# Optimization experiments

Measured on AMD Instinct MI355X. Metric: run time of the kernel, lower is better.

## Reference

```python
import jax, jax.numpy as jnp
import numpy as np

N = 50000       # nodes
E = 1600000     # edges (avg degree 32)
IN = 64         # in_channels
ED = 16         # edge_dim
H = 128         # hidden_channels


def setup_inputs() -> dict:
    key = jax.random.key(0)
    ks = jax.random.split(key, 32)
    rn = lambda k, shape, s: jax.random.normal(k, shape, jnp.float32) * s
    inp = {}
    inp['x'] = rn(ks[0], (N, IN), 1.0)
    inp['edge_index'] = jax.random.randint(ks[1], (2, E), 0, N, dtype=jnp.int64)
    inp['edge_attr'] = rn(ks[2], (E, ED), 1.0)
    # per-layer params: edge linear (ED -> node_dim), MLP (d_in->H, H->H)
    node_dims = [IN, H, H]
    i = 3
    for l, d in enumerate(node_dims):
        inp[f'We{l}'] = rn(ks[i], (ED, d), 1.0 / np.sqrt(ED)); i += 1
        inp[f'be{l}'] = jnp.zeros((d,), jnp.float32)
        inp[f'W1_{l}'] = rn(ks[i], (d, H), 1.0 / np.sqrt(d)); i += 1
        inp[f'b1_{l}'] = jnp.zeros((H,), jnp.float32)
        inp[f'W2_{l}'] = rn(ks[i], (H, H), 1.0 / np.sqrt(H)); i += 1
        inp[f'b2_{l}'] = jnp.zeros((H,), jnp.float32)
    inp['Wlin'] = rn(ks[i], (H, 1), 1.0 / np.sqrt(H))
    inp['blin'] = jnp.zeros((1,), jnp.float32)
    return inp


def gine_conv(x, src, dst, ea, We, be, W1, b1, W2, b2):
    # message: relu(x_j + Lin_e(edge_attr)); aggregate: sum into dst; eps=0
    msg = jax.nn.relu(x[src] + ea @ We + be)            # [E, d]
    agg = jax.ops.segment_sum(msg, dst, num_segments=x.shape[0])  # [N, d]
    h = x + agg                                          # (1+eps)*x + agg, eps=0
    return jax.nn.relu(h @ W1 + b1) @ W2 + b2            # MLP


def reference(x, edge_index, edge_attr,
              We0, be0, W1_0, b1_0, W2_0, b2_0,
              We1, be1, W1_1, b1_1, W2_1, b2_1,
              We2, be2, W1_2, b1_2, W2_2, b2_2,
              Wlin, blin):
    src, dst = edge_index[0], edge_index[1]
    h = jax.nn.relu(gine_conv(x, src, dst, edge_attr, We0, be0, W1_0, b1_0, W2_0, b2_0))
    h = jax.nn.relu(gine_conv(h, src, dst, edge_attr, We1, be1, W1_1, b1_1, W2_1, b2_1))
    h = jax.nn.relu(gine_conv(h, src, dst, edge_attr, We2, be2, W1_2, b1_2, W2_2, b2_2))
    out = jax.nn.sigmoid(h @ Wlin + blin)                # [N, 1]
    return out.squeeze(-1)                               # [N]
```

## Files before the change

### kernel.cpp

```cpp
#include <hip/hip_runtime.h>
#include <math.h>


#define BLK 256

typedef __attribute__((ext_vector_type(2))) float f32x2;

__device__ inline f32x2 pk_fma(f32x2 a, f32x2 b, f32x2 c) {
    f32x2 d;
    asm("v_pk_fma_f32 %0, %1, %2, %3" : "=v"(d) : "v"(a), "v"(b), "v"(c));
    return d;
}


__global__ void detect_kernel(const unsigned int* __restrict__ ei, int* __restrict__ flag) {
    int t = blockIdx.x * blockDim.x + threadIdx.x;
    if (t < 1024) {
        if (ei[2 * t + 1] != 0u) atomicOr(flag, 1);
    }
}

__global__ void convert_hist_kernel(const int* __restrict__ ei32, const long long* __restrict__ ei64,
                                    const int* __restrict__ flag, int E,
                                    int* __restrict__ src, int* __restrict__ dst,
                                    int* __restrict__ counts) {
    int e = blockIdx.x * blockDim.x + threadIdx.x;
    if (e >= E) return;
    int s, d;
    if (*flag) { s = ei32[e]; d = ei32[E + e]; }
    else       { s = (int)ei64[e]; d = (int)ei64[E + e]; }
    src[e] = s; dst[e] = d;
    atomicAdd(&counts[d], 1);
}

__global__ void scan_kernel(const int* __restrict__ counts, int* __restrict__ offsets, int n) {
    __shared__ int tsum[256];
    __shared__ int texcl[256];
    int t = threadIdx.x;
    int chunk = (n + 255) >> 8;
    int b = t * chunk, e = min(b + chunk, n);
    int s = 0;
    for (int i = b; i < e; i++) s += counts[i];
    tsum[t] = s;
    __syncthreads();
    if (t == 0) {
        int run = 0;
        for (int i = 0; i < 256; i++) { texcl[i] = run; run += tsum[i]; }
        offsets[n] = run;
    }
    __syncthreads();
    int run = texcl[t];
    for (int i = b; i < e; i++) { offsets[i] = run; run += counts[i]; }
}

__global__ void scatter_ea_kernel(const int* __restrict__ src, const int* __restrict__ dst,
                                  const int* __restrict__ offsets, int* __restrict__ cursor,
                                  const float4* __restrict__ ea4,
                                  int* __restrict__ srcp, float4* __restrict__ eap4, int E) {
    int e = blockIdx.x * blockDim.x + threadIdx.x;
    if (e >= E) return;
    int d = dst[e];
    int pos = offsets[d] + atomicAdd(&cursor[d], 1);
    srcp[pos] = src[e];
    float4 a = ea4[(size_t)e * 4 + 0], b = ea4[(size_t)e * 4 + 1];
    float4 c = ea4[(size_t)e * 4 + 2], w = ea4[(size_t)e * 4 + 3];
    eap4[(size_t)pos * 4 + 0] = a;
    eap4[(size_t)pos * 4 + 1] = b;
    eap4[(size_t)pos * 4 + 2] = c;
    eap4[(size_t)pos * 4 + 3] = w;
}

template <int D>
__global__ __launch_bounds__(256) void aggregate_kernel(
    const float* __restrict__ x, const float* __restrict__ eap,
    const int* __restrict__ srcp,
    const float* __restrict__ We, const float* __restrict__ be,
    const int* __restrict__ offsets,
    float* __restrict__ h, int n) {
    constexpr int C = D / 64;
    int lane = threadIdx.x & 63;
    int node = __builtin_amdgcn_readfirstlane(blockIdx.x * 4 + (threadIdx.x >> 6));
    if (node >= n) return;
    int c0 = lane * C;

    f32x2 wp[C][8];
#pragma unroll
    for (int j = 0; j < C; j++)
#pragma unroll
        for (int t = 0; t < 8; t++) {
            f32x2 v; v.x = We[(2 * t) * D + c0 + j]; v.y = We[(2 * t + 1) * D + c0 + j];
            wp[j][t] = v;
        }
    float bias[C], acc[C];
#pragma unroll
    for (int j = 0; j < C; j++) {
        bias[j] = be[c0 + j];
        acc[j] = x[(size_t)node * D + c0 + j];
    }
    int p = offsets[node], pe = offsets[node + 1];

    for (; p + 4 <= pe; p += 4) {
        int s0 = srcp[p], s1 = srcp[p + 1], s2 = srcp[p + 2], s3 = srcp[p + 3];
        float xv[4][C];
        {
            const float* r0 = x + (size_t)s0 * D + c0;
            const float* r1 = x + (size_t)s1 * D + c0;
            const float* r2 = x + (size_t)s2 * D + c0;
            const float* r3 = x + (size_t)s3 * D + c0;
            if constexpr (C == 2) {
                float2 t0 = *(const float2*)r0, t1 = *(const float2*)r1;
                float2 t2 = *(const float2*)r2, t3 = *(const float2*)r3;
                xv[0][0] = t0.x; xv[0][1] = t0.y; xv[1][0] = t1.x; xv[1][1] = t1.y;
                xv[2][0] = t2.x; xv[2][1] = t2.y; xv[3][0] = t3.x; xv[3][1] = t3.y;
            } else {
                xv[0][0] = *r0; xv[1][0] = *r1; xv[2][0] = *r2; xv[3][0] = *r3;
            }
        }
#pragma unroll
        for (int u = 0; u < 4; u++) {
            const float4* er = (const float4*)(eap + (size_t)(p + u) * 16);
            float4 e0 = er[0], e1 = er[1], e2 = er[2], e3 = er[3];
            f32x2 ev[8];
            ev[0].x = e0.x; ev[0].y = e0.y;  ev[1].x = e0.z; ev[1].y = e0.w;
            ev[2].x = e1.x; ev[2].y = e1.y;  ev[3].x = e1.z; ev[3].y = e1.w;
            ev[4].x = e2.x; ev[4].y = e2.y;  ev[5].x = e2.z; ev[5].y = e2.w;
            ev[6].x = e3.x; ev[6].y = e3.y;  ev[7].x = e3.z; ev[7].y = e3.w;
#pragma unroll
            for (int j = 0; j < C; j++) {
                f32x2 prod; prod.x = xv[u][j] + bias[j]; prod.y = 0.f;
#pragma unroll
                for (int t = 0; t < 8; t++) prod = pk_fma(ev[t], wp[j][t], prod);
                acc[j] += fmaxf(prod.x + prod.y, 0.f);
            }
        }
    }
    for (; p < pe; p++) {
        int s = srcp[p];
        const float* xr = x + (size_t)s * D + c0;
        float xv[C];
        if constexpr (C == 2) { float2 t = *(const float2*)xr; xv[0] = t.x; xv[1] = t.y; }
        else xv[0] = *xr;
        const float4* er = (const float4*)(eap + (size_t)p * 16);
        float4 e0 = er[0], e1 = er[1], e2 = er[2], e3 = er[3];
        f32x2 ev[8];
        ev[0].x = e0.x; ev[0].y = e0.y;  ev[1].x = e0.z; ev[1].y = e0.w;
        ev[2].x = e1.x; ev[2].y = e1.y;  ev[3].x = e1.z; ev[3].y = e1.w;
        ev[4].x = e2.x; ev[4].y = e2.y;  ev[5].x = e2.z; ev[5].y = e2.w;
        ev[6].x = e3.x; ev[6].y = e3.y;  ev[7].x = e3.z; ev[7].y = e3.w;
#pragma unroll
        for (int j = 0; j < C; j++) {
            f32x2 prod; prod.x = xv[j] + bias[j]; prod.y = 0.f;
#pragma unroll
            for (int t = 0; t < 8; t++) prod = pk_fma(ev[t], wp[j][t], prod);
            acc[j] += fmaxf(prod.x + prod.y, 0.f);
        }
    }
#pragma unroll
    for (int j = 0; j < C; j++) h[(size_t)node * D + c0 + j] = acc[j];
}

template <int K>
__global__ __launch_bounds__(256) void gemm_kernel(
    const float* __restrict__ A, const float* __restrict__ B,
    const float* __restrict__ bias, float* __restrict__ C, int n) {
    __shared__ __align__(16) float As[16][68];
    __shared__ __align__(16) float Bs[16][128];
    int t = threadIdx.x;
    int row0 = blockIdx.x * 64;
    int tr = t >> 5, tc = t & 31;
    float acc[8][4];
#pragma unroll
    for (int r = 0; r < 8; r++)
#pragma unroll
        for (int c = 0; c < 4; c++) acc[r][c] = 0.f;

    int lr = t >> 2, lk = (t & 3) * 4;
    int bk = t >> 4, bc = (t & 15) * 8;

    for (int ks = 0; ks < K; ks += 16) {
        float4 a;
        int grow = row0 + lr;
        if (grow < n) a = *(const float4*)(A + (size_t)grow * K + ks + lk);
        else a = make_float4(0.f, 0.f, 0.f, 0.f);
        As[lk + 0][lr] = a.x; As[lk + 1][lr] = a.y;
        As[lk + 2][lr] = a.z; As[lk + 3][lr] = a.w;

        const float4* bp = (const float4*)(B + (size_t)(ks + bk) * 128 + bc);
        float4 b0 = bp[0], b1 = bp[1];
        *(float4*)&Bs[bk][bc] = b0;
        *(float4*)&Bs[bk][bc + 4] = b1;
        __syncthreads();
#pragma unroll
        for (int kk = 0; kk < 16; kk++) {
            float4 a0 = *(const float4*)&As[kk][tr * 8];
            float4 a1 = *(const float4*)&As[kk][tr * 8 + 4];
            float4 bv = *(const float4*)&Bs[kk][tc * 4];
            float ar[8] = {a0.x, a0.y, a0.z, a0.w, a1.x, a1.y, a1.z, a1.w};
            float bc4[4] = {bv.x, bv.y, bv.z, bv.w};
#pragma unroll
            for (int r = 0; r < 8; r++)
#pragma unroll
                for (int c = 0; c < 4; c++) acc[r][c] = fmaf(ar[r], bc4[c], acc[r][c]);
        }
        __syncthreads();
    }
    float4 bb = *(const float4*)(bias + tc * 4);
#pragma unroll
    for (int r = 0; r < 8; r++) {
        int grow = row0 + tr * 8 + r;
        if (grow < n) {
            float4 v;
            v.x = fmaxf(acc[r][0] + bb.x, 0.f);
            v.y = fmaxf(acc[r][1] + bb.y, 0.f);
            v.z = fmaxf(acc[r][2] + bb.z, 0.f);
            v.w = fmaxf(acc[r][3] + bb.w, 0.f);
            *(float4*)(C + (size_t)grow * 128 + tc * 4) = v;
        }
    }
}

__global__ __launch_bounds__(256) void final_kernel(
    const float* __restrict__ x, const float* __restrict__ Wlin,
    const float* __restrict__ blin, float* __restrict__ out, int n) {
    int lane = threadIdx.x & 63;
    int node = blockIdx.x * 4 + (threadIdx.x >> 6);
    if (node >= n) return;
    float2 w = *(const float2*)(Wlin + lane * 2);
    float2 xv = *(const float2*)(x + (size_t)node * 128 + lane * 2);
    float v = xv.x * w.x + xv.y * w.y;
#pragma unroll
    for (int off = 32; off; off >>= 1) v += __shfl_down(v, off, 64);
    if (lane == 0) out[node] = 1.f / (1.f + expf(-(v + blin[0])));
}

extern "C" void kernel_launch(void* const* d_in, const int* in_sizes, int n_in,
                              void* d_out, int out_size, void* d_ws, size_t ws_size,
                              hipStream_t stream) {
    const float* x_in = (const float*)d_in[0];
    const void* ei    = d_in[1];
    const float* ea   = (const float*)d_in[2];
    const float* We[3]  = {(const float*)d_in[3], (const float*)d_in[9],  (const float*)d_in[15]};
    const float* be[3]  = {(const float*)d_in[4], (const float*)d_in[10], (const float*)d_in[16]};
    const float* W1[3]  = {(const float*)d_in[5], (const float*)d_in[11], (const float*)d_in[17]};
    const float* b1[3]  = {(const float*)d_in[6], (const float*)d_in[12], (const float*)d_in[18]};
    const float* W2[3]  = {(const float*)d_in[7], (const float*)d_in[13], (const float*)d_in[19]};
    const float* b2[3]  = {(const float*)d_in[8], (const float*)d_in[14], (const float*)d_in[20]};
    const float* Wlin = (const float*)d_in[21];
    const float* blin = (const float*)d_in[22];
    float* out = (float*)d_out;

    const int N = in_sizes[0] / 64;
    const int E = in_sizes[1] / 2;

    size_t off = 0;
    auto alloc = [&](size_t bytes) {
        void* p = (char*)d_ws + off;
        off += (bytes + 255) & ~(size_t)255;
        return p;
    };
    int*   flag    = (int*)alloc(4);
    int*   src32   = (int*)alloc((size_t)E * 4);
    int*   dst32   = (int*)alloc((size_t)E * 4);
    int*   counts  = (int*)alloc((size_t)N * 4);
    int*   offsets = (int*)alloc((size_t)(N + 1) * 4);
    int*   cursor  = (int*)alloc((size_t)N * 4);
    int*   srcp    = (int*)alloc((size_t)E * 4);
    float* eap     = (float*)alloc((size_t)E * 16 * 4);
    float* bufA    = (float*)alloc((size_t)N * 128 * 4);
    float* bufB    = (float*)alloc((size_t)N * 128 * 4);
    float* bufC    = (float*)alloc((size_t)N * 128 * 4);

    hipMemsetAsync(flag, 0, 4, stream);
    hipMemsetAsync(counts, 0, (size_t)N * 4, stream);
    hipMemsetAsync(cursor, 0, (size_t)N * 4, stream);

    int egrid = (E + BLK - 1) / BLK;
    detect_kernel<<<4, BLK, 0, stream>>>((const unsigned int*)ei, flag);
    convert_hist_kernel<<<egrid, BLK, 0, stream>>>((const int*)ei, (const long long*)ei, flag, E,
                                                   src32, dst32, counts);
    scan_kernel<<<1, BLK, 0, stream>>>(counts, offsets, N);
    scatter_ea_kernel<<<egrid, BLK, 0, stream>>>(src32, dst32, offsets, cursor,
                                                 (const float4*)ea, srcp, (float4*)eap, E);

    int ngrid4 = (N + 3) / 4;
    int ggrid  = (N + 63) / 64;

    aggregate_kernel<64><<<ngrid4, BLK, 0, stream>>>(x_in, eap, srcp, We[0], be[0], offsets, bufA, N);
    gemm_kernel<64><<<ggrid, BLK, 0, stream>>>(bufA, W1[0], b1[0], bufB, N);
    gemm_kernel<128><<<ggrid, BLK, 0, stream>>>(bufB, W2[0], b2[0], bufC, N);
    aggregate_kernel<128><<<ngrid4, BLK, 0, stream>>>(bufC, eap, srcp, We[1], be[1], offsets, bufA, N);
    gemm_kernel<128><<<ggrid, BLK, 0, stream>>>(bufA, W1[1], b1[1], bufB, N);
    gemm_kernel<128><<<ggrid, BLK, 0, stream>>>(bufB, W2[1], b2[1], bufC, N);
    aggregate_kernel<128><<<ngrid4, BLK, 0, stream>>>(bufC, eap, srcp, We[2], be[2], offsets, bufA, N);
    gemm_kernel<128><<<ggrid, BLK, 0, stream>>>(bufA, W1[2], b1[2], bufB, N);
    gemm_kernel<128><<<ggrid, BLK, 0, stream>>>(bufB, W2[2], b2[2], bufC, N);

    final_kernel<<<ngrid4, BLK, 0, stream>>>(bufC, Wlin, blin, out, N);
}
```

Before: 987.6 us.

## Fuse MLP GEMMs via LDS, split edge permutation, unroll aggregation by eight

Fuses the two per-layer GEMMs into one kernel that keeps the hidden activation tile in shared memory, avoiding a global write and read of an N x 128 buffer per layer. The edge-attribute scatter is split into a position pass storing (src, edge id) pairs and a separate coalesced gather pass that permutes edge attributes. The aggregation loop is unrolled to eight edges to expose more outstanding gather loads. The larger LDS footprint may reduce occupancy of the fused MLP kernel, and the extra unrolling raises register pressure.

```diff
diff --git a/kernel.cpp b/kernel.cpp
--- a/kernel.cpp
+++ b/kernel.cpp
@@ -53,21 +53,25 @@
     for (int i = b; i < e; i++) { offsets[i] = run; run += counts[i]; }
 }
 
-__global__ void scatter_ea_kernel(const int* __restrict__ src, const int* __restrict__ dst,
-                                  const int* __restrict__ offsets, int* __restrict__ cursor,
-                                  const float4* __restrict__ ea4,
-                                  int* __restrict__ srcp, float4* __restrict__ eap4, int E) {
+__global__ void scatter_pos_kernel(const int* __restrict__ src, const int* __restrict__ dst,
+                                   const int* __restrict__ offsets, int* __restrict__ cursor,
+                                   int2* __restrict__ meta, int E) {
     int e = blockIdx.x * blockDim.x + threadIdx.x;
     if (e >= E) return;
     int d = dst[e];
     int pos = offsets[d] + atomicAdd(&cursor[d], 1);
-    srcp[pos] = src[e];
-    float4 a = ea4[(size_t)e * 4 + 0], b = ea4[(size_t)e * 4 + 1];
-    float4 c = ea4[(size_t)e * 4 + 2], w = ea4[(size_t)e * 4 + 3];
-    eap4[(size_t)pos * 4 + 0] = a;
-    eap4[(size_t)pos * 4 + 1] = b;
-    eap4[(size_t)pos * 4 + 2] = c;
-    eap4[(size_t)pos * 4 + 3] = w;
+    meta[pos] = make_int2(src[e], e);
+}
+
+__global__ void permute_gather_kernel(const int2* __restrict__ meta,
+                                      const float4* __restrict__ ea4,
+                                      int* __restrict__ srcp, float4* __restrict__ eap4, int E) {
+    int t = blockIdx.x * blockDim.x + threadIdx.x;
+    if (t >= E * 4) return;
+    int pos = t >> 2, c = t & 3;
+    int2 m = meta[pos];
+    eap4[(size_t)pos * 4 + c] = ea4[(size_t)m.y * 4 + c];
+    if (c == 0) srcp[pos] = m.x;
 }
 
 template <int D>
@@ -99,25 +103,19 @@
     }
     int p = offsets[node], pe = offsets[node + 1];
 
-    for (; p + 4 <= pe; p += 4) {
-        int s0 = srcp[p], s1 = srcp[p + 1], s2 = srcp[p + 2], s3 = srcp[p + 3];
-        float xv[4][C];
-        {
-            const float* r0 = x + (size_t)s0 * D + c0;
-            const float* r1 = x + (size_t)s1 * D + c0;
-            const float* r2 = x + (size_t)s2 * D + c0;
-            const float* r3 = x + (size_t)s3 * D + c0;
-            if constexpr (C == 2) {
-                float2 t0 = *(const float2*)r0, t1 = *(const float2*)r1;
-                float2 t2 = *(const float2*)r2, t3 = *(const float2*)r3;
-                xv[0][0] = t0.x; xv[0][1] = t0.y; xv[1][0] = t1.x; xv[1][1] = t1.y;
-                xv[2][0] = t2.x; xv[2][1] = t2.y; xv[3][0] = t3.x; xv[3][1] = t3.y;
-            } else {
-                xv[0][0] = *r0; xv[1][0] = *r1; xv[2][0] = *r2; xv[3][0] = *r3;
-            }
-        }
-#pragma unroll
-        for (int u = 0; u < 4; u++) {
+    for (; p + 8 <= pe; p += 8) {
+        int s[8];
+#pragma unroll
+        for (int u = 0; u < 8; u++) s[u] = srcp[p + u];
+        float xv[8][C];
+#pragma unroll
+        for (int u = 0; u < 8; u++) {
+            const float* r = x + (size_t)s[u] * D + c0;
+            if constexpr (C == 2) { float2 tv = *(const float2*)r; xv[u][0] = tv.x; xv[u][1] = tv.y; }
+            else xv[u][0] = *r;
+        }
+#pragma unroll
+        for (int u = 0; u < 8; u++) {
             const float4* er = (const float4*)(eap + (size_t)(p + u) * 16);
             float4 e0 = er[0], e1 = er[1], e2 = er[2], e3 = er[3];
             f32x2 ev[8];
@@ -160,11 +158,13 @@
 }
 
 template <int K>
-__global__ __launch_bounds__(256) void gemm_kernel(
-    const float* __restrict__ A, const float* __restrict__ B,
-    const float* __restrict__ bias, float* __restrict__ C, int n) {
+__global__ __launch_bounds__(256) void mlp_kernel(
+    const float* __restrict__ A, const float* __restrict__ W1, const float* __restrict__ b1,
+    const float* __restrict__ W2, const float* __restrict__ b2,
+    float* __restrict__ C, int n) {
     __shared__ __align__(16) float As[16][68];
     __shared__ __align__(16) float Bs[16][128];
+    __shared__ __align__(16) float Ts[64][132];
     int t = threadIdx.x;
     int row0 = blockIdx.x * 64;
     int tr = t >> 5, tc = t & 31;
@@ -185,10 +185,10 @@
         As[lk + 0][lr] = a.x; As[lk + 1][lr] = a.y;
         As[lk + 2][lr] = a.z; As[lk + 3][lr] = a.w;
 
-        const float4* bp = (const float4*)(B + (size_t)(ks + bk) * 128 + bc);
-        float4 b0 = bp[0], b1 = bp[1];
+        const float4* bp = (const float4*)(W1 + (size_t)(ks + bk) * 128 + bc);
+        float4 b0 = bp[0], b1v = bp[1];
         *(float4*)&Bs[bk][bc] = b0;
-        *(float4*)&Bs[bk][bc + 4] = b1;
+        *(float4*)&Bs[bk][bc + 4] = b1v;
         __syncthreads();
 #pragma unroll
         for (int kk = 0; kk < 16; kk++) {
@@ -204,7 +204,43 @@
         }
         __syncthreads();
     }
-    float4 bb = *(const float4*)(bias + tc * 4);
+    {
+        float4 bb = *(const float4*)(b1 + tc * 4);
+#pragma unroll
+        for (int r = 0; r < 8; r++) {
+            Ts[tr * 8 + r][tc * 4 + 0] = fmaxf(acc[r][0] + bb.x, 0.f);
+            Ts[tr * 8 + r][tc * 4 + 1] = fmaxf(acc[r][1] + bb.y, 0.f);
+            Ts[tr * 8 + r][tc * 4 + 2] = fmaxf(acc[r][2] + bb.z, 0.f);
+            Ts[tr * 8 + r][tc * 4 + 3] = fmaxf(acc[r][3] + bb.w, 0.f);
+        }
+    }
+    __syncthreads();
+
+#pragma unroll
+    for (int r = 0; r < 8; r++)
+#pragma unroll
+        for (int c = 0; c < 4; c++) acc[r][c] = 0.f;
+    for (int ks = 0; ks < 128; ks += 16) {
+        const float4* bp = (const float4*)(W2 + (size_t)(ks + bk) * 128 + bc);
+        float4 b0 = bp[0], b1v = bp[1];
+        *(float4*)&Bs[bk][bc] = b0;
+        *(float4*)&Bs[bk][bc + 4] = b1v;
+        __syncthreads();
+#pragma unroll
+        for (int kk = 0; kk < 16; kk++) {
+            float4 bv = *(const float4*)&Bs[kk][tc * 4];
+            float bc4[4] = {bv.x, bv.y, bv.z, bv.w};
+            float ar[8];
+#pragma unroll
+            for (int r = 0; r < 8; r++) ar[r] = Ts[tr * 8 + r][ks + kk];
+#pragma unroll
+            for (int r = 0; r < 8; r++)
+#pragma unroll
+                for (int c = 0; c < 4; c++) acc[r][c] = fmaf(ar[r], bc4[c], acc[r][c]);
+        }
+        __syncthreads();
+    }
+    float4 bb = *(const float4*)(b2 + tc * 4);
 #pragma unroll
     for (int r = 0; r < 8; r++) {
         int grow = row0 + tr * 8 + r;
@@ -264,10 +300,10 @@
     int*   counts  = (int*)alloc((size_t)N * 4);
     int*   offsets = (int*)alloc((size_t)(N + 1) * 4);
     int*   cursor  = (int*)alloc((size_t)N * 4);
+    int2*  meta    = (int2*)alloc((size_t)E * 8);
     int*   srcp    = (int*)alloc((size_t)E * 4);
     float* eap     = (float*)alloc((size_t)E * 16 * 4);
     float* bufA    = (float*)alloc((size_t)N * 128 * 4);
-    float* bufB    = (float*)alloc((size_t)N * 128 * 4);
     float* bufC    = (float*)alloc((size_t)N * 128 * 4);
 
     hipMemsetAsync(flag, 0, 4, stream);
@@ -279,21 +315,19 @@
     convert_hist_kernel<<<egrid, BLK, 0, stream>>>((const int*)ei, (const long long*)ei, flag, E,
                                                    src32, dst32, counts);
     scan_kernel<<<1, BLK, 0, stream>>>(counts, offsets, N);
-    scatter_ea_kernel<<<egrid, BLK, 0, stream>>>(src32, dst32, offsets, cursor,
-                                                 (const float4*)ea, srcp, (float4*)eap, E);
+    scatter_pos_kernel<<<egrid, BLK, 0, stream>>>(src32, dst32, offsets, cursor, meta, E);
+    permute_gather_kernel<<<(E * 4 + BLK - 1) / BLK, BLK, 0, stream>>>(
+        meta, (const float4*)ea, srcp, (float4*)eap, E);
 
     int ngrid4 = (N + 3) / 4;
     int ggrid  = (N + 63) / 64;
 
     aggregate_kernel<64><<<ngrid4, BLK, 0, stream>>>(x_in, eap, srcp, We[0], be[0], offsets, bufA, N);
-    gemm_kernel<64><<<ggrid, BLK, 0, stream>>>(bufA, W1[0], b1[0], bufB, N);
-    gemm_kernel<128><<<ggrid, BLK, 0, stream>>>(bufB, W2[0], b2[0], bufC, N);
+    mlp_kernel<64><<<ggrid, BLK, 0, stream>>>(bufA, W1[0], b1[0], W2[0], b2[0], bufC, N);
     aggregate_kernel<128><<<ngrid4, BLK, 0, stream>>>(bufC, eap, srcp, We[1], be[1], offsets, bufA, N);
-    gemm_kernel<128><<<ggrid, BLK, 0, stream>>>(bufA, W1[1], b1[1], bufB, N);
-    gemm_kernel<128><<<ggrid, BLK, 0, stream>>>(bufB, W2[1], b2[1], bufC, N);
+    mlp_kernel<128><<<ggrid, BLK, 0, stream>>>(bufA, W1[1], b1[1], W2[1], b2[1], bufC, N);
     aggregate_kernel<128><<<ngrid4, BLK, 0, stream>>>(bufC, eap, srcp, We[2], be[2], offsets, bufA, N);
-    gemm_kernel<128><<<ggrid, BLK, 0, stream>>>(bufA, W1[2], b1[2], bufB, N);
-    gemm_kernel<128><<<ggrid, BLK, 0, stream>>>(bufB, W2[2], b2[2], bufC, N);
+    mlp_kernel<128><<<ggrid, BLK, 0, stream>>>(bufA, W1[2], b1[2], W2[2], b2[2], bufC, N);
 
     final_kernel<<<ngrid4, BLK, 0, stream>>>(bufC, Wlin, blin, out, N);
 }
```

New measurement: 1.040 ms. +5.3%, slower.
